# Kernel optimization log

Hardware: AMD Instinct MI355X
Metric: run time of the kernel (lower is better)

## Reference

```python
import jax, jax.numpy as jnp
import numpy as np

MAX_POS = float(2 ** 20)  # max_position_encoding_distance
B, C, S = 2, 1536, 16384
H, T, P = 768, 367, 128
NUM_ORG = 2


def _apply_rope(x, positions):
    # x: (B, P, T, H), positions: (B, P) int -> rotate pairs (first-half, second-half)
    half = x.shape[-1] // 2
    inv_freq = 1.0 / (MAX_POS ** (jnp.arange(half, dtype=jnp.float32) / half))  # (half,)
    ang = positions.astype(jnp.float32)[:, :, None, None] * inv_freq  # (B, P, 1, half)
    cos, sin = jnp.cos(ang), jnp.sin(ang)
    x1, x2 = x[..., :half], x[..., half:]
    return jnp.concatenate([x1 * cos - x2 * sin, x1 * sin + x2 * cos], axis=-1)


def _gather_affine_rope(logits, idx, params, organism_index):
    # logits: (B, H, S); idx: (B, P); params: (ORG, 2, T, H)
    bi = jnp.arange(logits.shape[0])[:, None]
    x = logits[bi, :, idx]  # (B, P, H)
    bp = params[organism_index]  # (B, 2, T, H)
    scale = bp[:, 0][:, None]   # (B, 1, T, H)
    offset = bp[:, 1][:, None]  # (B, 1, T, H)
    x = scale * x[:, :, None, :] + offset  # (B, P, T, H)
    return _apply_rope(x, idx)


def setup_inputs() -> dict:
    key = jax.random.key(0)
    ks = jax.random.split(key, 9)
    stdv = 1.0 / np.sqrt(C)
    return {
        'embeddings_1bp': jax.random.normal(ks[0], (B, C, S), jnp.float32),
        'conv_w': jax.random.normal(ks[1], (NUM_ORG, H, C), jnp.float32) * stdv,
        'conv_b': jax.random.normal(ks[2], (NUM_ORG, H), jnp.float32) * 0.02,
        'rope_pos_donor': jax.random.normal(ks[3], (NUM_ORG, 2, T, H), jnp.float32) * 0.05,
        'rope_pos_acceptor': jax.random.normal(ks[4], (NUM_ORG, 2, T, H), jnp.float32) * 0.05,
        'rope_neg_donor': jax.random.normal(ks[5], (NUM_ORG, 2, T, H), jnp.float32) * 0.05,
        'rope_neg_acceptor': jax.random.normal(ks[6], (NUM_ORG, 2, T, H), jnp.float32) * 0.05,
        'organism_index': jax.random.randint(ks[7], (B,), 0, NUM_ORG),
        'splice_site_positions': jax.random.randint(ks[8], (B, 4, P), 0, S),
    }


def reference(embeddings_1bp, conv_w, conv_b, rope_pos_donor, rope_pos_acceptor,
              rope_neg_donor, rope_neg_acceptor, organism_index, splice_site_positions):
    pos_d, pos_a = splice_site_positions[:, 0], splice_site_positions[:, 1]
    neg_d, neg_a = splice_site_positions[:, 2], splice_site_positions[:, 3]

    # organism-indexed 1x1 conv: (B,C,S) x (B,H,C) -> (B,H,S)
    w = conv_w[organism_index]
    b = conv_b[organism_index]
    logits = jnp.einsum('bcs,boc->bos', embeddings_1bp, w) + b[:, :, None]

    pdl = _gather_affine_rope(logits, pos_d, rope_pos_donor, organism_index)
    pal = _gather_affine_rope(logits, pos_a, rope_pos_acceptor, organism_index)
    ndl = _gather_affine_rope(logits, neg_d, rope_neg_donor, organism_index)
    nal = _gather_affine_rope(logits, neg_a, rope_neg_acceptor, organism_index)

    pos_counts = jax.nn.softplus(jnp.einsum('bdth,bath->bdat', pdl, pal))  # (B,P,P,T)
    neg_counts = jax.nn.softplus(jnp.einsum('bdth,bath->bdat', ndl, nal))

    pos_mask = (pos_d >= 0)[:, :, None] & (pos_a >= 0)[:, None, :]  # (B,P,P)
    neg_mask = (neg_d >= 0)[:, :, None] & (neg_a >= 0)[:, None, :]
    # tissue_mask: default num_tracks_per_organism -> all True
    tissue_mask = jnp.ones((B, T), dtype=bool)
    pos_mask = pos_mask[:, :, :, None] & tissue_mask[:, None, None, :]
    neg_mask = neg_mask[:, :, :, None] & tissue_mask[:, None, None, :]

    junction_mask = jnp.concatenate([pos_mask, neg_mask], axis=-1)  # (B,P,P,2T)
    pred_counts = jnp.concatenate([pos_counts, neg_counts], axis=-1)
    pred_counts = jnp.where(junction_mask, pred_counts, 0.0)
    return pred_counts, junction_mask
```

## Files before the change

### kernel.cpp

```cpp
#include <hip/hip_runtime.h>
#include <hip/hip_bf16.h>
#include <math.h>
#include <string.h>

#define B_    2
#define C_    1536
#define S_    16384
#define H_    768
#define T_    367
#define P_    128
#define HALF_ 384
#define TT_   734
#define NT2_  184
#define PRED_ELEMS 24051712

#define XHH_OFF  0
#define CSH_OFF  393216
#define INVF_OFF 786432
#define XCB_OFF  787200

typedef short short8 __attribute__((ext_vector_type(8)));
typedef _Float16 f16x8 __attribute__((ext_vector_type(8)));
typedef _Float16 h2    __attribute__((ext_vector_type(2)));
typedef float f32x4  __attribute__((ext_vector_type(4)));

__device__ __forceinline__ unsigned int packbf2(float a, float b) {
    __hip_bfloat162 h = __float22bfloat162_rn(make_float2(a, b));
    unsigned int r; __builtin_memcpy(&r, &h, 4); return r;
}
__device__ __forceinline__ unsigned short packbf1(float a) {
    __hip_bfloat16 h = __float2bfloat16(a);
    unsigned short r; __builtin_memcpy(&r, &h, 2); return r;
}
__device__ __forceinline__ unsigned short f2h(float x) {
    _Float16 h = (_Float16)x;
    unsigned short r; __builtin_memcpy(&r, &h, 2); return r;
}
__device__ __forceinline__ h2 bch(unsigned int v) { h2 r; __builtin_memcpy(&r, &v, 4); return r; }
__device__ __forceinline__ unsigned int hcb(h2 v) { unsigned int r; __builtin_memcpy(&r, &v, 4); return r; }

__global__ void gather_cols(const float* __restrict__ emb,
                            const int* __restrict__ sp,
                            unsigned short* __restrict__ xcb) {
    int blk = blockIdx.x;
    int p = blk & 127;
    int g = (blk >> 7) & 3;
    int b = blk >> 9;
    int s = sp[(b * 4 + g) * P_ + p];
    const float* src = emb + (size_t)b * C_ * S_ + s;
    unsigned short* dst = xcb + ((size_t)(b * 4 + g) * P_ + p) * C_;
    for (int c = threadIdx.x; c < C_; c += blockDim.x)
        dst[c] = packbf1(src[(size_t)c * S_]);
}

__global__ __launch_bounds__(256) void logits_mfma(
    const unsigned short* __restrict__ xcb, const float* __restrict__ w,
    const float* __restrict__ bias, const int* __restrict__ org,
    unsigned short* __restrict__ xhh) {
    __shared__ __align__(16) unsigned short tX[64 * 64];
    __shared__ __align__(16) unsigned short tW[64 * 64];
    int mt = blockIdx.x;
    int nt = blockIdx.y;
    int o = org[mt >> 3];
    int r0 = mt * 64, h0 = nt * 64;
    int tid = threadIdx.x;
    int lane = tid & 63, wid = tid >> 6;
    int wrow = (wid >> 1) * 32, wcol = (wid & 1) * 32;
    int lr = lane & 15, lq = lane >> 4;
    int gr0 = (lq ^ (lr & 7)) * 8;

    f32x4 acc[2][2];
    #pragma unroll
    for (int i = 0; i < 2; ++i)
        #pragma unroll
        for (int j = 0; j < 2; ++j) acc[i][j] = (f32x4){0.f, 0.f, 0.f, 0.f};

    int srow = tid >> 2, sg = tid & 3;

    for (int kc = 0; kc < C_; kc += 64) {
        if (kc) __syncthreads();
        {
            const unsigned short* src = xcb + (size_t)(r0 + srow) * C_ + kc;
            unsigned short* drow = tX + srow * 64;
            #pragma unroll
            for (int i = 0; i < 2; ++i) {
                int g = sg + i * 4;
                uint4 v = *(const uint4*)(src + g * 8);
                *(uint4*)&drow[(g ^ (srow & 7)) * 8] = v;
            }
        }
        {
            const float* srcw = w + ((size_t)o * H_ + h0 + srow) * C_ + kc;
            unsigned short* drow = tW + srow * 64;
            #pragma unroll
            for (int i = 0; i < 2; ++i) {
                int g = sg + i * 4;
                float4 v0 = *(const float4*)(srcw + g * 8);
                float4 v1 = *(const float4*)(srcw + g * 8 + 4);
                uint4 pk;
                pk.x = packbf2(v0.x, v0.y); pk.y = packbf2(v0.z, v0.w);
                pk.z = packbf2(v1.x, v1.y); pk.w = packbf2(v1.z, v1.w);
                *(uint4*)&drow[(g ^ (srow & 7)) * 8] = pk;
            }
        }
        __syncthreads();
        #pragma unroll
        for (int kk = 0; kk < 64; kk += 32) {
            short8 af[2], bf2[2];
            #pragma unroll
            for (int fi = 0; fi < 2; ++fi)
                af[fi] = *(const short8*)&tX[(wrow + fi * 16 + lr) * 64 + (gr0 ^ kk)];
            #pragma unroll
            for (int fj = 0; fj < 2; ++fj)
                bf2[fj] = *(const short8*)&tW[(wcol + fj * 16 + lr) * 64 + (gr0 ^ kk)];
            #pragma unroll
            for (int fi = 0; fi < 2; ++fi)
                #pragma unroll
                for (int fj = 0; fj < 2; ++fj)
                    acc[fi][fj] = __builtin_amdgcn_mfma_f32_16x16x32_bf16(
                        af[fi], bf2[fj], acc[fi][fj], 0, 0, 0);
        }
    }
    #pragma unroll
    for (int fi = 0; fi < 2; ++fi)
        #pragma unroll
        for (int rr = 0; rr < 4; ++rr) {
            int r = r0 + wrow + fi * 16 + lq * 4 + rr;
            #pragma unroll
            for (int fj = 0; fj < 2; ++fj) {
                int h = h0 + wcol + fj * 16 + lr;
                int hj = (h < HALF_) ? h : (h - HALF_);
                int sel = (h < HALF_) ? 0 : 1;
                xhh[(size_t)r * H_ + (hj >> 2) * 8 + sel * 4 + (hj & 3)] =
                    f2h(acc[fi][fj][rr] + bias[o * H_ + h]);
            }
        }
}

__global__ void init_invf(double* __restrict__ invf) {
    int j = threadIdx.x;
    if (j < HALF_) invf[j] = exp2(-20.0 * (double)j / 384.0);
}

__global__ void rope_table(const int* __restrict__ sp,
                           const double* __restrict__ invf,
                           unsigned short* __restrict__ csh) {
    int e = blockIdx.x * blockDim.x + threadIdx.x;
    if (e >= B_ * 4 * P_ * HALF_) return;
    int j = e % HALF_;
    int r = e / HALF_;
    int s = sp[r];
    const double TWO_PI = 6.283185307179586476925286766559;
    double ang = (double)s * invf[j];
    double k = rint(ang * (1.0 / TWO_PI));
    float fr = (float)(ang - k * TWO_PI);
    float sv, cv;
    __sincosf(fr, &sv, &cv);
    int base = r * H_ + (j >> 2) * 8 + (j & 3);
    csh[base]     = f2h(cv);
    csh[base + 4] = f2h(sv);
}

__global__ __launch_bounds__(1024, 4) void junction_mfma(
    const unsigned short* __restrict__ xhh, const unsigned short* __restrict__ csh,
    const float* __restrict__ rpd, const float* __restrict__ rpa,
    const float* __restrict__ rnd, const float* __restrict__ rna,
    const int* __restrict__ org, const int* __restrict__ sp,
    unsigned short* __restrict__ w1) {
    __shared__ __align__(16) unsigned short smem[65536];
    __shared__ __align__(16) unsigned short scofh[6144];
    __shared__ int vD[P_], vA[P_];

    int nwg = gridDim.x;
    int orig = blockIdx.x;
    int xcd = orig & 7;
    int q = nwg >> 3, r8 = nwg & 7;
    int blk = (xcd < r8 ? xcd * (q + 1) : r8 * (q + 1) + (xcd - r8) * q) + (orig >> 3);

    int tp = blk % NT2_;
    int sign = (blk / NT2_) & 1;
    int b = blk / (2 * NT2_);
    int o = org[b];
    int t0 = 2 * tp, t1 = t0 + 1;
    int t1ok = (t1 < T_);
    int t1c = t1ok ? t1 : t0;
    int gd = sign * 2, ga = sign * 2 + 1;
    const float* pd = sign ? rnd : rpd;
    const float* pa = sign ? rna : rpa;
    int tid = threadIdx.x;

    for (int e = tid; e < 6144; e += 1024) {
        int tsel = e / 3072;
        int rem = e - tsel * 3072;
        int side = rem / 1536;
        int rem2 = rem - side * 1536;
        int arr = rem2 / 768;
        int e2 = rem2 - arr * 768;
        int tt = tsel ? t1c : t0;
        const float* base = (side ? pa : pd) + ((size_t)(o * 2 + arr) * T_ + tt) * H_;
        int hj = (e2 < HALF_) ? e2 : (e2 - HALF_);
        int sel = (e2 < HALF_) ? 0 : 1;
        int pos = (hj >> 2) * 8 + sel * 4 + (hj & 3);
        scofh[((tsel * 2 + side) * 2 + arr) * 768 + pos] = f2h(base[e2]);
    }
    if (tid < P_) {
        vD[tid] = sp[(b * 4 + gd) * P_ + tid] >= 0;
        vA[tid] = sp[(b * 4 + ga) * P_ + tid] >= 0;
    }
    const unsigned short* xdh = xhh + ((size_t)(b * 4 + gd) * P_) * H_;
    const unsigned short* xah = xhh + ((size_t)(b * 4 + ga) * P_) * H_;
    const unsigned short* cdh = csh + ((size_t)(b * 4 + gd) * P_) * H_;
    const unsigned short* cah = csh + ((size_t)(b * 4 + ga) * P_) * H_;

    int lane = tid & 63, wid = tid >> 6;
    int wrow = (wid >> 2) * 32, wcol = (wid & 3) * 32;
    int lr = lane & 15, lq = lane >> 4;
    int gr0 = (lq ^ (lr & 7)) * 8;

    f32x4 a0[2][2], a1[2][2];
    #pragma unroll
    for (int i = 0; i < 2; ++i)
        #pragma unroll
        for (int j = 0; j < 2; ++j) {
            a0[i][j] = (f32x4){0.f, 0.f, 0.f, 0.f};
            a1[i][j] = (f32x4){0.f, 0.f, 0.f, 0.f};
        }

    __syncthreads();

    for (int ch = 0; ch < 12; ++ch) {
        unsigned short* bufb = smem + (ch & 1) * 32768;

        #pragma unroll
        for (int s = 0; s < 2; ++s) {
            int slot = tid + s * 1024;
            int row = slot >> 3, gran = slot & 7;
            int side = row >> 7, prow = row & 127;
            const unsigned short* xb = side ? xah : xdh;
            const unsigned short* cb = side ? cah : cdh;
            int off = prow * H_ + ch * 64 + gran * 8;
            uint4 xv = *(const uint4*)(xb + off);
            uint4 cv = *(const uint4*)(cb + off);
            int sw = prow * 64 + ((gran ^ (prow & 7)) << 3);
            int kb = (ch * 8 + gran) * 8;
            h2 cA = bch(cv.x), cB = bch(cv.y), sA = bch(cv.z), sB = bch(cv.w);
            {
                const unsigned short* cof = scofh + (side * 2) * 768;
                uint4 sc = *(const uint4*)(cof + kb);
                uint4 of = *(const uint4*)(cof + 768 + kb);
                h2 u1a = __builtin_elementwise_fma(bch(sc.x), bch(xv.x), bch(of.x));
                h2 u1b = __builtin_elementwise_fma(bch(sc.y), bch(xv.y), bch(of.y));
                h2 u2a = __builtin_elementwise_fma(bch(sc.z), bch(xv.z), bch(of.z));
                h2 u2b = __builtin_elementwise_fma(bch(sc.w), bch(xv.w), bch(of.w));
                uint4 wv;
                wv.x = hcb(__builtin_elementwise_fma(u1a, cA, -(u2a * sA)));
                wv.y = hcb(__builtin_elementwise_fma(u1b, cB, -(u2b * sB)));
                wv.z = hcb(__builtin_elementwise_fma(u1a, sA, u2a * cA));
                wv.w = hcb(__builtin_elementwise_fma(u1b, sB, u2b * cB));
                *(uint4*)&bufb[side * 8192 + sw] = wv;
            }
            {
                const unsigned short* cof = scofh + ((2 + side) * 2) * 768;
                uint4 sc = *(const uint4*)(cof + kb);
                uint4 of = *(const uint4*)(cof + 768 + kb);
                h2 u1a = __builtin_elementwise_fma(bch(sc.x), bch(xv.x), bch(of.x));
                h2 u1b = __builtin_elementwise_fma(bch(sc.y), bch(xv.y), bch(of.y));
                h2 u2a = __builtin_elementwise_fma(bch(sc.z), bch(xv.z), bch(of.z));
                h2 u2b = __builtin_elementwise_fma(bch(sc.w), bch(xv.w), bch(of.w));
                uint4 wv;
                wv.x = hcb(__builtin_elementwise_fma(u1a, cA, -(u2a * sA)));
                wv.y = hcb(__builtin_elementwise_fma(u1b, cB, -(u2b * sB)));
                wv.z = hcb(__builtin_elementwise_fma(u1a, sA, u2a * cA));
                wv.w = hcb(__builtin_elementwise_fma(u1b, sB, u2b * cB));
                *(uint4*)&bufb[16384 + side * 8192 + sw] = wv;
            }
        }
        __syncthreads();

        __builtin_amdgcn_s_setprio(1);
        {
            const unsigned short* tD = bufb;
            const unsigned short* tA = bufb + 8192;
            #pragma unroll
            for (int kk = 0; kk < 64; kk += 32) {
                f16x8 af[2], bf2[2];
                #pragma unroll
                for (int fi = 0; fi < 2; ++fi)
                    af[fi] = *(const f16x8*)&tD[(wrow + fi * 16 + lr) * 64 + (gr0 ^ kk)];
                #pragma unroll
                for (int fj = 0; fj < 2; ++fj)
                    bf2[fj] = *(const f16x8*)&tA[(wcol + fj * 16 + lr) * 64 + (gr0 ^ kk)];
                #pragma unroll
                for (int fi = 0; fi < 2; ++fi)
                    #pragma unroll
                    for (int fj = 0; fj < 2; ++fj)
                        a0[fi][fj] = __builtin_amdgcn_mfma_f32_16x16x32_f16(
                            af[fi], bf2[fj], a0[fi][fj], 0, 0, 0);
            }
        }
        {
            const unsigned short* tD = bufb + 16384;
            const unsigned short* tA = bufb + 24576;
            #pragma unroll
            for (int kk = 0; kk < 64; kk += 32) {
                f16x8 af[2], bf2[2];
                #pragma unroll
                for (int fi = 0; fi < 2; ++fi)
                    af[fi] = *(const f16x8*)&tD[(wrow + fi * 16 + lr) * 64 + (gr0 ^ kk)];
                #pragma unroll
                for (int fj = 0; fj < 2; ++fj)
                    bf2[fj] = *(const f16x8*)&tA[(wcol + fj * 16 + lr) * 64 + (gr0 ^ kk)];
                #pragma unroll
                for (int fi = 0; fi < 2; ++fi)
                    #pragma unroll
                    for (int fj = 0; fj < 2; ++fj)
                        a1[fi][fj] = __builtin_amdgcn_mfma_f32_16x16x32_f16(
                            af[fi], bf2[fj], a1[fi][fj], 0, 0, 0);
            }
        }
        __builtin_amdgcn_s_setprio(0);
    }

    #pragma unroll
    for (int fi = 0; fi < 2; ++fi) {
        #pragma unroll
        for (int rr = 0; rr < 4; ++rr) {
            int d = wrow + fi * 16 + lq * 4 + rr;
            int vd = vD[d];
            #pragma unroll
            for (int fj = 0; fj < 2; ++fj) {
                int a = wcol + fj * 16 + lr;
                int va = vA[a];
                float x0 = a0[fi][fj][rr];
                float v0 = 0.0f;
                if (vd && va) v0 = (x0 > 15.0f) ? x0 : __logf(1.0f + __expf(x0));
                smem[d * P_ + a] = packbf1(v0);
                float x1 = a1[fi][fj][rr];
                float v1 = 0.0f;
                if (vd && va) v1 = (x1 > 15.0f) ? x1 : __logf(1.0f + __expf(x1));
                smem[16384 + d * P_ + a] = packbf1(v1);
            }
        }
    }
    __syncthreads();
    const uint4* s4 = (const uint4*)smem;
    uint4* d40 = (uint4*)(w1 + (size_t)((b * 2 + sign) * T_ + t0) * (P_ * P_));
    for (int i = tid; i < 2048; i += 1024) d40[i] = s4[i];
    if (t1ok) {
        uint4* d41 = (uint4*)(w1 + (size_t)((b * 2 + sign) * T_ + t1) * (P_ * P_));
        for (int i = tid; i < 2048; i += 1024) d41[i] = s4[2048 + i];
    }
}

__global__ __launch_bounds__(256) void transpose_out(const __hip_bfloat16* __restrict__ w1,
                                                     float* __restrict__ pred) {
    __shared__ float tile[64 * 129];
    int blk = blockIdx.x;
    int tt = blk % 6;
    int d = (blk / 6) % P_;
    int bs = blk / (6 * P_);
    int b = bs >> 1, sign = bs & 1;
    int t0 = tt * 64;
    int tcnt = min(64, T_ - t0);
    int tid = threadIdx.x;

    const __hip_bfloat16* src = w1 + (size_t)bs * T_ * P_ * P_ + (size_t)d * P_;
    for (int e = tid; e < tcnt * P_; e += 256) {
        int i = e >> 7, a = e & 127;
        tile[i * 129 + a] = __bfloat162float(src[(size_t)(t0 + i) * P_ * P_ + a]);
    }
    __syncthreads();
    float* dst = pred + ((size_t)(b * P_ + d) * P_) * TT_ + sign * T_ + t0;
    for (int e = tid; e < P_ * 64; e += 256) {
        int a = e >> 6, ii = e & 63;
        if (ii < tcnt) dst[(size_t)a * TT_ + ii] = tile[ii * 129 + a];
    }
}

__global__ void mask_fill(const int* __restrict__ sp, float* __restrict__ mask) {
    int blk = blockIdx.x;
    int a = blk & 127;
    int d = (blk >> 7) & 127;
    int b = blk >> 14;
    bool vp = (sp[(b * 4 + 0) * P_ + d] >= 0) && (sp[(b * 4 + 1) * P_ + a] >= 0);
    bool vn = (sp[(b * 4 + 2) * P_ + d] >= 0) && (sp[(b * 4 + 3) * P_ + a] >= 0);
    float* dst = mask + (size_t)blk * TT_;
    for (int st = threadIdx.x; st < TT_; st += blockDim.x)
        dst[st] = (st < T_ ? vp : vn) ? 1.0f : 0.0f;
}

extern "C" void kernel_launch(void* const* d_in, const int* in_sizes, int n_in,
                              void* d_out, int out_size, void* d_ws, size_t ws_size,
                              hipStream_t stream) {
    const float* emb  = (const float*)d_in[0];
    const float* w    = (const float*)d_in[1];
    const float* bias = (const float*)d_in[2];
    const float* rpd  = (const float*)d_in[3];
    const float* rpa  = (const float*)d_in[4];
    const float* rnd  = (const float*)d_in[5];
    const float* rna  = (const float*)d_in[6];
    const int*   org  = (const int*)d_in[7];
    const int*   sp   = (const int*)d_in[8];

    float* out = (float*)d_out;
    float* ws  = (float*)d_ws;
    unsigned short* xhh = (unsigned short*)(ws + XHH_OFF);
    unsigned short* csh = (unsigned short*)(ws + CSH_OFF);
    double* invf = (double*)(ws + INVF_OFF);
    unsigned short* xcb = (unsigned short*)(ws + XCB_OFF);
    float* pred  = out;
    float* maskp = out + PRED_ELEMS;
    unsigned short* w1 = (unsigned short*)maskp;

    init_invf<<<1, 384, 0, stream>>>(invf);
    gather_cols<<<1024, 256, 0, stream>>>(emb, sp, xcb);
    rope_table<<<1536, 256, 0, stream>>>(sp, invf, csh);
    dim3 gl(16, 12);
    logits_mfma<<<gl, 256, 0, stream>>>(xcb, w, bias, org, xhh);
    junction_mfma<<<2 * 2 * NT2_, 1024, 0, stream>>>(xhh, csh, rpd, rpa, rnd, rna, org, sp, w1);
    transpose_out<<<2 * 2 * P_ * 6, 256, 0, stream>>>((const __hip_bfloat16*)w1, pred);
    mask_fill<<<32768, 256, 0, stream>>>(sp, maskp);
}
```

Measured before the change: 214.5 us.

## Halve junction block size, single-buffer LDS, fuse mask write into transpose

The junction kernel now runs with 512 threads per block, each wave covering 64 rows instead of 32. It uses a single LDS staging buffer with an extra barrier per chunk, which halves shared memory and may allow more blocks per CU, at the cost of losing overlap between chunks. When the workspace is large enough, the bf16 intermediate lives in the workspace instead of aliasing the mask output. A new finalize kernel then writes the transposed predictions and the mask in one pass, replacing the separate mask_fill launch and its extra traversal of the output.

Result: slower. 244.2 us (+13.9%).

```diff
diff --git a/kernel.cpp b/kernel.cpp
--- a/kernel.cpp
+++ b/kernel.cpp
@@ -18,6 +18,7 @@
 #define CSH_OFF  393216
 #define INVF_OFF 786432
 #define XCB_OFF  787200
+#define W1WS_OFF 1573632
 
 typedef short short8 __attribute__((ext_vector_type(8)));
 typedef _Float16 f16x8 __attribute__((ext_vector_type(8)));
@@ -161,13 +162,13 @@
     csh[base + 4] = f2h(sv);
 }
 
-__global__ __launch_bounds__(1024, 4) void junction_mfma(
+__global__ __launch_bounds__(512, 4) void junction_mfma(
     const unsigned short* __restrict__ xhh, const unsigned short* __restrict__ csh,
     const float* __restrict__ rpd, const float* __restrict__ rpa,
     const float* __restrict__ rnd, const float* __restrict__ rna,
     const int* __restrict__ org, const int* __restrict__ sp,
     unsigned short* __restrict__ w1) {
-    __shared__ __align__(16) unsigned short smem[65536];
+    __shared__ __align__(16) unsigned short smem[32768];
     __shared__ __align__(16) unsigned short scofh[6144];
     __shared__ int vD[P_], vA[P_];
 
@@ -189,7 +190,7 @@
     const float* pa = sign ? rna : rpa;
     int tid = threadIdx.x;
 
-    for (int e = tid; e < 6144; e += 1024) {
+    for (int e = tid; e < 6144; e += 512) {
         int tsel = e / 3072;
         int rem = e - tsel * 3072;
         int side = rem / 1536;
@@ -213,13 +214,13 @@
     const unsigned short* cah = csh + ((size_t)(b * 4 + ga) * P_) * H_;
 
     int lane = tid & 63, wid = tid >> 6;
-    int wrow = (wid >> 2) * 32, wcol = (wid & 3) * 32;
+    int wrow = (wid >> 2) * 64, wcol = (wid & 3) * 32;
     int lr = lane & 15, lq = lane >> 4;
     int gr0 = (lq ^ (lr & 7)) * 8;
 
-    f32x4 a0[2][2], a1[2][2];
+    f32x4 a0[4][2], a1[4][2];
     #pragma unroll
-    for (int i = 0; i < 2; ++i)
+    for (int i = 0; i < 4; ++i)
         #pragma unroll
         for (int j = 0; j < 2; ++j) {
             a0[i][j] = (f32x4){0.f, 0.f, 0.f, 0.f};
@@ -229,11 +230,11 @@
     __syncthreads();
 
     for (int ch = 0; ch < 12; ++ch) {
-        unsigned short* bufb = smem + (ch & 1) * 32768;
-
-        #pragma unroll
-        for (int s = 0; s < 2; ++s) {
-            int slot = tid + s * 1024;
+        if (ch) __syncthreads();
+
+        #pragma unroll
+        for (int s = 0; s < 4; ++s) {
+            int slot = tid + s * 512;
             int row = slot >> 3, gran = slot & 7;
             int side = row >> 7, prow = row & 127;
             const unsigned short* xb = side ? xah : xdh;
@@ -245,7 +246,7 @@
             int kb = (ch * 8 + gran) * 8;
             h2 cA = bch(cv.x), cB = bch(cv.y), sA = bch(cv.z), sB = bch(cv.w);
             {
-                const unsigned short* cof = scofh + (side * 2) * 768;
+                const unsigned short* cof = scofh + side * 1536;
                 uint4 sc = *(const uint4*)(cof + kb);
                 uint4 of = *(const uint4*)(cof + 768 + kb);
                 h2 u1a = __builtin_elementwise_fma(bch(sc.x), bch(xv.x), bch(of.x));
@@ -257,10 +258,10 @@
                 wv.y = hcb(__builtin_elementwise_fma(u1b, cB, -(u2b * sB)));
                 wv.z = hcb(__builtin_elementwise_fma(u1a, sA, u2a * cA));
                 wv.w = hcb(__builtin_elementwise_fma(u1b, sB, u2b * cB));
-                *(uint4*)&bufb[side * 8192 + sw] = wv;
+                *(uint4*)&smem[side * 8192 + sw] = wv;
             }
             {
-                const unsigned short* cof = scofh + ((2 + side) * 2) * 768;
+                const unsigned short* cof = scofh + (2 + side) * 1536;
                 uint4 sc = *(const uint4*)(cof + kb);
                 uint4 of = *(const uint4*)(cof + 768 + kb);
                 h2 u1a = __builtin_elementwise_fma(bch(sc.x), bch(xv.x), bch(of.x));
@@ -272,26 +273,26 @@
                 wv.y = hcb(__builtin_elementwise_fma(u1b, cB, -(u2b * sB)));
                 wv.z = hcb(__builtin_elementwise_fma(u1a, sA, u2a * cA));
                 wv.w = hcb(__builtin_elementwise_fma(u1b, sB, u2b * cB));
-                *(uint4*)&bufb[16384 + side * 8192 + sw] = wv;
+                *(uint4*)&smem[16384 + side * 8192 + sw] = wv;
             }
         }
         __syncthreads();
 
         __builtin_amdgcn_s_setprio(1);
         {
-            const unsigned short* tD = bufb;
-            const unsigned short* tA = bufb + 8192;
+            const unsigned short* tD = smem;
+            const unsigned short* tA = smem + 8192;
             #pragma unroll
             for (int kk = 0; kk < 64; kk += 32) {
-                f16x8 af[2], bf2[2];
-                #pragma unroll
-                for (int fi = 0; fi < 2; ++fi)
+                f16x8 af[4], bf2[2];
+                #pragma unroll
+                for (int fi = 0; fi < 4; ++fi)
                     af[fi] = *(const f16x8*)&tD[(wrow + fi * 16 + lr) * 64 + (gr0 ^ kk)];
                 #pragma unroll
                 for (int fj = 0; fj < 2; ++fj)
                     bf2[fj] = *(const f16x8*)&tA[(wcol + fj * 16 + lr) * 64 + (gr0 ^ kk)];
                 #pragma unroll
-                for (int fi = 0; fi < 2; ++fi)
+                for (int fi = 0; fi < 4; ++fi)
                     #pragma unroll
                     for (int fj = 0; fj < 2; ++fj)
                         a0[fi][fj] = __builtin_amdgcn_mfma_f32_16x16x32_f16(
@@ -299,19 +300,19 @@
             }
         }
         {
-            const unsigned short* tD = bufb + 16384;
-            const unsigned short* tA = bufb + 24576;
+            const unsigned short* tD = smem + 16384;
+            const unsigned short* tA = smem + 24576;
             #pragma unroll
             for (int kk = 0; kk < 64; kk += 32) {
-                f16x8 af[2], bf2[2];
-                #pragma unroll
-                for (int fi = 0; fi < 2; ++fi)
+                f16x8 af[4], bf2[2];
+                #pragma unroll
+                for (int fi = 0; fi < 4; ++fi)
                     af[fi] = *(const f16x8*)&tD[(wrow + fi * 16 + lr) * 64 + (gr0 ^ kk)];
                 #pragma unroll
                 for (int fj = 0; fj < 2; ++fj)
                     bf2[fj] = *(const f16x8*)&tA[(wcol + fj * 16 + lr) * 64 + (gr0 ^ kk)];
                 #pragma unroll
-                for (int fi = 0; fi < 2; ++fi)
+                for (int fi = 0; fi < 4; ++fi)
                     #pragma unroll
                     for (int fj = 0; fj < 2; ++fj)
                         a1[fi][fj] = __builtin_amdgcn_mfma_f32_16x16x32_f16(
@@ -321,8 +322,9 @@
         __builtin_amdgcn_s_setprio(0);
     }
 
+    __syncthreads();
     #pragma unroll
-    for (int fi = 0; fi < 2; ++fi) {
+    for (int fi = 0; fi < 4; ++fi) {
         #pragma unroll
         for (int rr = 0; rr < 4; ++rr) {
             int d = wrow + fi * 16 + lq * 4 + rr;
@@ -345,10 +347,48 @@
     __syncthreads();
     const uint4* s4 = (const uint4*)smem;
     uint4* d40 = (uint4*)(w1 + (size_t)((b * 2 + sign) * T_ + t0) * (P_ * P_));
-    for (int i = tid; i < 2048; i += 1024) d40[i] = s4[i];
+    for (int i = tid; i < 2048; i += 512) d40[i] = s4[i];
     if (t1ok) {
         uint4* d41 = (uint4*)(w1 + (size_t)((b * 2 + sign) * T_ + t1) * (P_ * P_));
-        for (int i = tid; i < 2048; i += 1024) d41[i] = s4[2048 + i];
+        for (int i = tid; i < 2048; i += 512) d41[i] = s4[2048 + i];
+    }
+}
+
+__global__ __launch_bounds__(256) void finalize_ws(const __hip_bfloat16* __restrict__ w1,
+                                                   const int* __restrict__ sp,
+                                                   float* __restrict__ pred,
+                                                   float* __restrict__ mask) {
+    __shared__ float tile[64 * 129];
+    __shared__ float mval[P_];
+    int blk = blockIdx.x;
+    int tt = blk % 6;
+    int d = (blk / 6) % P_;
+    int bs = blk / (6 * P_);
+    int b = bs >> 1, sign = bs & 1;
+    int t0 = tt * 64;
+    int tcnt = min(64, T_ - t0);
+    int tid = threadIdx.x;
+
+    const __hip_bfloat16* src = w1 + (size_t)bs * T_ * P_ * P_ + (size_t)d * P_;
+    for (int e = tid; e < tcnt * P_; e += 256) {
+        int i = e >> 7, a = e & 127;
+        tile[i * 129 + a] = __bfloat162float(src[(size_t)(t0 + i) * P_ * P_ + a]);
+    }
+    if (tid < P_) {
+        bool vd = sp[(b * 4 + sign * 2) * P_ + d] >= 0;
+        bool va = sp[(b * 4 + sign * 2 + 1) * P_ + tid] >= 0;
+        mval[tid] = (vd && va) ? 1.0f : 0.0f;
+    }
+    __syncthreads();
+    size_t obase = ((size_t)(b * P_ + d) * P_) * TT_ + sign * T_ + t0;
+    float* dstp = pred + obase;
+    float* dstm = mask + obase;
+    for (int e = tid; e < P_ * 64; e += 256) {
+        int a = e >> 6, ii = e & 63;
+        if (ii < tcnt) {
+            dstp[(size_t)a * TT_ + ii] = tile[ii * 129 + a];
+            dstm[(size_t)a * TT_ + ii] = mval[a];
+        }
     }
 }
 
@@ -410,14 +450,23 @@
     unsigned short* xcb = (unsigned short*)(ws + XCB_OFF);
     float* pred  = out;
     float* maskp = out + PRED_ELEMS;
-    unsigned short* w1 = (unsigned short*)maskp;
+
+    size_t w1_bytes = (size_t)4 * T_ * P_ * P_ * 2;
+    size_t need = (size_t)W1WS_OFF * 4 + w1_bytes;
+    bool ws_ok = (ws_size >= need);
+    unsigned short* w1 = ws_ok ? (unsigned short*)(ws + W1WS_OFF)
+                               : (unsigned short*)maskp;
 
     init_invf<<<1, 384, 0, stream>>>(invf);
     gather_cols<<<1024, 256, 0, stream>>>(emb, sp, xcb);
     rope_table<<<1536, 256, 0, stream>>>(sp, invf, csh);
     dim3 gl(16, 12);
     logits_mfma<<<gl, 256, 0, stream>>>(xcb, w, bias, org, xhh);
-    junction_mfma<<<2 * 2 * NT2_, 1024, 0, stream>>>(xhh, csh, rpd, rpa, rnd, rna, org, sp, w1);
-    transpose_out<<<2 * 2 * P_ * 6, 256, 0, stream>>>((const __hip_bfloat16*)w1, pred);
-    mask_fill<<<32768, 256, 0, stream>>>(sp, maskp);
-}
+    junction_mfma<<<2 * 2 * NT2_, 512, 0, stream>>>(xhh, csh, rpd, rpa, rnd, rna, org, sp, w1);
+    if (ws_ok) {
+        finalize_ws<<<2 * 2 * P_ * 6, 256, 0, stream>>>((const __hip_bfloat16*)w1, sp, pred, maskp);
+    } else {
+        transpose_out<<<2 * 2 * P_ * 6, 256, 0, stream>>>((const __hip_bfloat16*)w1, pred);
+        mask_fill<<<32768, 256, 0, stream>>>(sp, maskp);
+    }
+}
```
